# Performance work log

Measured on AMD Instinct MI355X. Metric: run time of the kernel, lower is better.

## Reference

```python
import jax, jax.numpy as jnp
import numpy as np

B, T, C = 2, 2048, 1024
NH = 16
HD = C // NH

def setup_inputs() -> dict:
    key = jax.random.key(0)
    k1, k2, k3 = jax.random.split(key, 3)
    x = jax.random.normal(k1, (B, T, C), dtype=jnp.float32)
    w_attn = jax.random.normal(k2, (C, 3 * C), dtype=jnp.float32) * 0.02
    w_proj = jax.random.normal(k3, (C, C), dtype=jnp.float32) * 0.02
    return {"x": x, "w_attn": w_attn, "w_proj": w_proj}

def reference(x, w_attn, w_proj):
    b, t, c = x.shape
    qkv = x @ w_attn                                  # [B,T,3C]
    q, k, v = jnp.split(qkv, 3, axis=-1)
    # [B,NH,T,HD]
    q = q.reshape(b, t, NH, HD).transpose(0, 2, 1, 3)
    k = k.reshape(b, t, NH, HD).transpose(0, 2, 1, 3)
    v = v.reshape(b, t, NH, HD).transpose(0, 2, 1, 3)
    scale = 1.0 / np.sqrt(HD).astype(np.float32)
    att = jnp.einsum('bhqd,bhkd->bhqk', q, k) * scale  # [B,NH,T,T]
    causal = jnp.tril(jnp.ones((t, t), dtype=bool))
    att = jnp.where(causal[None, None], att, jnp.float32(-jnp.inf))
    att = jax.nn.softmax(att, axis=-1)
    y = jnp.einsum('bhqk,bhkd->bhqd', att, v)          # [B,NH,T,HD]
    y = y.transpose(0, 2, 1, 3).reshape(b, t, c)
    return y @ w_proj
```

## Files before the change

kernel.cpp:

```cpp
#include <hip/hip_runtime.h>
#include <hip/hip_bf16.h>

#define BB 2
#define TT 2048
#define CCH 1024
#define NHH 16
#define HDD 64
#define M_TOK (BB*TT)
#define N_QKV (3*CCH)

typedef __attribute__((ext_vector_type(8))) short bf16x8;
typedef __attribute__((ext_vector_type(4))) float f32x4;
typedef unsigned short u16;
typedef unsigned int u32;

__device__ __forceinline__ u16 f2bf(float f) {
    union { float f; u32 u; } v; v.f = f;
    u32 u = v.u;
    u32 r = (u + 0x7FFFu + ((u >> 16) & 1u)) >> 16;
    return (u16)r;
}

__device__ __forceinline__ u32 pk_bf16(float a, float b) {
    u32 ua = __float_as_uint(a) + 0x8000u;
    u32 ub = __float_as_uint(b) + 0x8000u;
    return __builtin_amdgcn_perm(ub, ua, 0x07060302u);
}

__device__ __forceinline__ void async_copy16(const void* g, void* l) {
    __builtin_amdgcn_global_load_lds((__attribute__((address_space(1))) void*)g,
                                     (__attribute__((address_space(3))) void*)l,
                                     16, 0, 0);
}


__global__ __launch_bounds__(256) void cast_bf16_kernel(
    const float* __restrict__ src, u16* __restrict__ dst, int n4) {
    int i = blockIdx.x * 256 + threadIdx.x;
    if (i < n4) {
        float4 f = ((const float4*)src)[i];
        ushort4 o;
        o.x = f2bf(f.x); o.y = f2bf(f.y); o.z = f2bf(f.z); o.w = f2bf(f.w);
        ((ushort4*)dst)[i] = o;
    }
}

__global__ __launch_bounds__(256) void transpose_bf16_kernel(
    const float* __restrict__ src, u16* __restrict__ dst, int R, int Cn,
    int scale_rows, float sc) {
    __shared__ float tile[32][33];
    int c0 = blockIdx.x * 32, r0 = blockIdx.y * 32;
    int tx = threadIdx.x, ty = threadIdx.y;
#pragma unroll
    for (int i = ty; i < 32; i += 8)
        tile[i][tx] = src[(size_t)(r0 + i) * Cn + c0 + tx];
    __syncthreads();
#pragma unroll
    for (int i = ty; i < 32; i += 8) {
        float v = tile[tx][i];
        if (c0 + i < scale_rows) v *= sc;
        dst[(size_t)(c0 + i) * R + r0 + tx] = f2bf(v);
    }
}


#define QKV_NK 16
#define QKV_AS_HALF 16384
#define QKV_BS_HALF 12288
#define QKV_SMEM_BYTES ((2*QKV_AS_HALF + 2*QKV_BS_HALF) * 2)

__global__ __launch_bounds__(512, 1) void qkv_gemm_kernel(
    const u16* __restrict__ A, const u16* __restrict__ Bt,
    u16* __restrict__ Qo, u16* __restrict__ Ko, u16* __restrict__ Vto)
{
    extern __shared__ __align__(16) u16 smem[];
    u16* AsB = smem;
    u16* BsB = smem + 2 * QKV_AS_HALF;
    int t = threadIdx.x;
    int lane = t & 63, w = t >> 6;
    int m0 = blockIdx.y * 256, n0 = blockIdx.x * 192;
    int mw = (w >> 1) * 64, nw = (w & 1) * 96;
    int mr = lane & 15, quad = lane >> 4, swm = mr & 7;

    f32x4 zero = {0.f, 0.f, 0.f, 0.f};
    f32x4 acc[4][6];
#pragma unroll
    for (int i = 0; i < 4; ++i)
#pragma unroll
        for (int j = 0; j < 6; ++j) acc[i][j] = zero;

    int lr = lane >> 3;
    int cswz = (lane & 7) ^ lr;
    const u16* gA[4]; int lAo[4];
#pragma unroll
    for (int p = 0; p < 4; ++p) {
        int grp = w * 4 + p;
        gA[p] = A + (size_t)(m0 + grp * 8 + lr) * CCH + cswz * 8;
        lAo[p] = (grp * 64 + lane) * 8;
    }
    const u16* gB[3]; int lBo[3];
#pragma unroll
    for (int p = 0; p < 3; ++p) {
        int grp = w * 3 + p;
        gB[p] = Bt + (size_t)(n0 + grp * 8 + lr) * CCH + cswz * 8;
        lBo[p] = (grp * 64 + lane) * 8;
    }

#define QKV_STAGE(K0, BUF) do {                                               \
    u16* dA_ = AsB + (BUF) * QKV_AS_HALF;                                     \
    u16* dB_ = BsB + (BUF) * QKV_BS_HALF;                                     \
    _Pragma("unroll") for (int p_ = 0; p_ < 4; ++p_)                          \
        async_copy16(gA[p_] + (K0), dA_ + lAo[p_]);                           \
    _Pragma("unroll") for (int p_ = 0; p_ < 3; ++p_)                          \
        async_copy16(gB[p_] + (K0), dB_ + lBo[p_]);                           \
  } while (0)

    QKV_STAGE(0, 0);
    QKV_STAGE(64, 1);

    for (int k = 0; k < QKV_NK; ++k) {
        int cur = k & 1;
        if (k == QKV_NK - 1) asm volatile("s_waitcnt vmcnt(0)" ::: "memory");
        else                 asm volatile("s_waitcnt vmcnt(7)" ::: "memory");
        __builtin_amdgcn_s_barrier();
        asm volatile("" ::: "memory");
        const u16* Ac = AsB + cur * QKV_AS_HALF;
        const u16* Bc = BsB + cur * QKV_BS_HALF;
        bf16x8 a0[4], a1[4], b0[6], b1[6];
#pragma unroll
        for (int i = 0; i < 4; ++i) {
            int r = (mw + i * 16 + mr) * 64;
            a0[i] = *(const bf16x8*)&Ac[r + ((quad ^ swm) << 3)];
            a1[i] = *(const bf16x8*)&Ac[r + (((quad + 4) ^ swm) << 3)];
        }
#pragma unroll
        for (int j = 0; j < 6; ++j) {
            int r = (nw + j * 16 + mr) * 64;
            b0[j] = *(const bf16x8*)&Bc[r + ((quad ^ swm) << 3)];
            b1[j] = *(const bf16x8*)&Bc[r + (((quad + 4) ^ swm) << 3)];
        }
#pragma unroll
        for (int i = 0; i < 4; ++i)
#pragma unroll
            for (int j = 0; j < 6; ++j)
                acc[i][j] = __builtin_amdgcn_mfma_f32_16x16x32_bf16(b0[j], a0[i], acc[i][j], 0, 0, 0);
        asm volatile("s_waitcnt lgkmcnt(0)" ::: "memory");
        __builtin_amdgcn_sched_barrier(0);
        __builtin_amdgcn_s_barrier();
        asm volatile("" ::: "memory");
        if (k < QKV_NK - 2) QKV_STAGE((k + 2) * 64, cur);
#pragma unroll
        for (int i = 0; i < 4; ++i)
#pragma unroll
            for (int j = 0; j < 6; ++j)
                acc[i][j] = __builtin_amdgcn_mfma_f32_16x16x32_bf16(b1[j], a1[i], acc[i][j], 0, 0, 0);
    }
#undef QKV_STAGE

#pragma unroll
    for (int i = 0; i < 4; ++i)
#pragma unroll
        for (int j = 0; j < 6; ++j) {
            int tok = m0 + mw + i * 16 + mr;
            int cg0 = n0 + nw + j * 16 + quad * 4;
            int part = cg0 >> 10;
            int cc = cg0 & 1023;
            int h = cc >> 6, d0 = cc & 63;
            int b = tok >> 11, tt = tok & 2047;
            int bh = b * NHH + h;
            if (part < 2) {
                u16* dstp = part ? Ko : Qo;
                uint2 o;
                o.x = pk_bf16(acc[i][j][0], acc[i][j][1]);
                o.y = pk_bf16(acc[i][j][2], acc[i][j][3]);
                *(uint2*)&dstp[((size_t)bh * TT + tt) * HDD + d0] = o;
            } else {
#pragma unroll
                for (int r = 0; r < 4; ++r)
                    Vto[((size_t)bh * HDD + d0 + r) * TT + tt] = f2bf(acc[i][j][r]);
            }
        }
}


#define PRJ_NK 16
#define PRJ_AS_HALF 8192
#define PRJ_SMEM_BYTES (4 * PRJ_AS_HALF * 2)

__global__ __launch_bounds__(512, 1) void proj_gemm_kernel(
    const u16* __restrict__ A, const u16* __restrict__ Bt, float* __restrict__ Cout)
{
    extern __shared__ __align__(16) u16 psmem[];
    u16* AsB = psmem;
    u16* BsB = psmem + 2 * PRJ_AS_HALF;
    int t = threadIdx.x;
    int lane = t & 63, w = t >> 6;
    int m0 = blockIdx.y * 128, n0 = blockIdx.x * 128;
    int mw = (w >> 1) * 32, nw = (w & 1) * 64;
    int mr = lane & 15, quad = lane >> 4, swm = mr & 7;

    f32x4 zero = {0.f, 0.f, 0.f, 0.f};
    f32x4 acc[2][4];
#pragma unroll
    for (int i = 0; i < 2; ++i)
#pragma unroll
        for (int j = 0; j < 4; ++j) acc[i][j] = zero;

    int lr = lane >> 3;
    int cswz = (lane & 7) ^ lr;
    const u16* gA[2]; int lAo[2];
#pragma unroll
    for (int p = 0; p < 2; ++p) {
        int grp = w * 2 + p;
        gA[p] = A + (size_t)(m0 + grp * 8 + lr) * CCH + cswz * 8;
        lAo[p] = (grp * 64 + lane) * 8;
    }
    const u16* gB[2]; int lBo[2];
#pragma unroll
    for (int p = 0; p < 2; ++p) {
        int grp = w * 2 + p;
        gB[p] = Bt + (size_t)(n0 + grp * 8 + lr) * CCH + cswz * 8;
        lBo[p] = (grp * 64 + lane) * 8;
    }

#define PRJ_STAGE(K0, BUF) do {                                               \
    u16* dA_ = AsB + (BUF) * PRJ_AS_HALF;                                     \
    u16* dB_ = BsB + (BUF) * PRJ_AS_HALF;                                     \
    _Pragma("unroll") for (int p_ = 0; p_ < 2; ++p_)                          \
        async_copy16(gA[p_] + (K0), dA_ + lAo[p_]);                           \
    _Pragma("unroll") for (int p_ = 0; p_ < 2; ++p_)                          \
        async_copy16(gB[p_] + (K0), dB_ + lBo[p_]);                           \
  } while (0)

    PRJ_STAGE(0, 0);
    PRJ_STAGE(64, 1);

    for (int k = 0; k < PRJ_NK; ++k) {
        int cur = k & 1;
        if (k == PRJ_NK - 1) asm volatile("s_waitcnt vmcnt(0)" ::: "memory");
        else                 asm volatile("s_waitcnt vmcnt(4)" ::: "memory");
        __builtin_amdgcn_s_barrier();
        asm volatile("" ::: "memory");
        const u16* Ac = AsB + cur * PRJ_AS_HALF;
        const u16* Bc = BsB + cur * PRJ_AS_HALF;
        bf16x8 a0[2], a1[2], b0[4], b1[4];
#pragma unroll
        for (int i = 0; i < 2; ++i) {
            int r = (mw + i * 16 + mr) * 64;
            a0[i] = *(const bf16x8*)&Ac[r + ((quad ^ swm) << 3)];
            a1[i] = *(const bf16x8*)&Ac[r + (((quad + 4) ^ swm) << 3)];
        }
#pragma unroll
        for (int j = 0; j < 4; ++j) {
            int r = (nw + j * 16 + mr) * 64;
            b0[j] = *(const bf16x8*)&Bc[r + ((quad ^ swm) << 3)];
            b1[j] = *(const bf16x8*)&Bc[r + (((quad + 4) ^ swm) << 3)];
        }
#pragma unroll
        for (int i = 0; i < 2; ++i)
#pragma unroll
            for (int j = 0; j < 4; ++j)
                acc[i][j] = __builtin_amdgcn_mfma_f32_16x16x32_bf16(b0[j], a0[i], acc[i][j], 0, 0, 0);
        asm volatile("s_waitcnt lgkmcnt(0)" ::: "memory");
        __builtin_amdgcn_sched_barrier(0);
        __builtin_amdgcn_s_barrier();
        asm volatile("" ::: "memory");
        if (k < PRJ_NK - 2) PRJ_STAGE((k + 2) * 64, cur);
#pragma unroll
        for (int i = 0; i < 2; ++i)
#pragma unroll
            for (int j = 0; j < 4; ++j)
                acc[i][j] = __builtin_amdgcn_mfma_f32_16x16x32_bf16(b1[j], a1[i], acc[i][j], 0, 0, 0);
    }
#undef PRJ_STAGE

#pragma unroll
    for (int i = 0; i < 2; ++i)
#pragma unroll
        for (int j = 0; j < 4; ++j) {
            int tok = m0 + mw + i * 16 + mr;
            int cg0 = n0 + nw + j * 16 + quad * 4;
            float4 v;
            v.x = acc[i][j][0]; v.y = acc[i][j][1];
            v.z = acc[i][j][2]; v.w = acc[i][j][3];
            *(float4*)&Cout[(size_t)tok * CCH + cg0] = v;
        }
}


#define PST2 40

template<bool MASK>
__device__ __forceinline__ void tile3(
    const u16* __restrict__ Kb, const u16* __restrict__ Vb, u16* __restrict__ pb,
    bf16x8 qf0, bf16x8 qf1, bf16x8 ones, int m, int quad, int sw, int kh,
    int kvb, int qcol, f32x4 (&o)[4], f32x4& lacc)
{
    f32x4 zero = {0.f, 0.f, 0.f, 0.f};
#pragma unroll
    for (int kc = 0; kc < 2; ++kc) {
        int rr = kh * 32 + kc * 16 + m;
        bf16x8 kf0 = *(const bf16x8*)&Kb[rr * 64 + ((quad ^ sw) << 3)];
        bf16x8 kf1 = *(const bf16x8*)&Kb[rr * 64 + (((quad + 4) ^ sw) << 3)];
        f32x4 s  = __builtin_amdgcn_mfma_f32_16x16x32_bf16(kf0, qf0, zero, 0, 0, 0);
        f32x4 st = __builtin_amdgcn_mfma_f32_16x16x32_bf16(kf1, qf1, s, 0, 0, 0);
        float e0, e1, e2, e3;
#pragma unroll
        for (int r = 0; r < 4; ++r) {
            float v = st[r];
            if (MASK && (kvb + kc * 16 + quad * 4 + r > qcol)) v = -1e30f;
            float e = __builtin_amdgcn_exp2f(v);
            if (r == 0) e0 = e; else if (r == 1) e1 = e; else if (r == 2) e2 = e; else e3 = e;
        }
        uint2 pk; pk.x = pk_bf16(e0, e1); pk.y = pk_bf16(e2, e3);
        *(uint2*)&pb[m * PST2 + kc * 16 + quad * 4] = pk;
    }
    bf16x8 pf = *(const bf16x8*)&pb[m * PST2 + quad * 8];
    lacc = __builtin_amdgcn_mfma_f32_16x16x32_bf16(ones, pf, lacc, 0, 0, 0);
#pragma unroll
    for (int dg = 0; dg < 4; ++dg) {
        int rr = dg * 16 + m;
        bf16x8 vf = *(const bf16x8*)&Vb[rr * 64 + (((kh * 4 + quad) ^ sw) << 3)];
        o[dg] = __builtin_amdgcn_mfma_f32_16x16x32_bf16(vf, pf, o[dg], 0, 0, 0);
    }
}

#define SM_U16 26880

__global__ __launch_bounds__(512, 2) void attn_kernel(
    const u16* __restrict__ Q, const u16* __restrict__ K,
    const u16* __restrict__ Vt, u16* __restrict__ Y)
{
    __shared__ __align__(16) u16 smem[SM_U16];
    int t = threadIdx.x;
    int w = t >> 6, lane = t & 63;
    int m = lane & 15, quad = lane >> 4;
    int iq = w >> 1, kh = w & 1;

    int bid = blockIdx.x;
    int head = bid & 31;
    int g = bid >> 5;
    int pr = (g < 8) ? g : 23 - g;
    int qbA = pr;
    int qbB = 31 - pr;
    int rbA = qbA * 64 + iq * 16;
    int rbB = qbB * 64 + iq * 16;

    const u16* qpA = Q + ((size_t)head * TT + rbA + m) * HDD + quad * 8;
    const u16* qpB = Q + ((size_t)head * TT + rbB + m) * HDD + quad * 8;
    bf16x8 qA0 = *(const bf16x8*)qpA;
    bf16x8 qA1 = *(const bf16x8*)(qpA + 32);
    bf16x8 qB0 = *(const bf16x8*)qpB;
    bf16x8 qB1 = *(const bf16x8*)(qpB + 32);

    bf16x8 ones;
#pragma unroll
    for (int i = 0; i < 8; ++i) ones[i] = (short)0x3F80;

    const u16* kbase = K + (size_t)head * TT * HDD;
    const u16* vbase = Vt + (size_t)head * HDD * TT;
    u16* pbA = smem + 16384 + (w * 2 + 0) * (16 * PST2);
    u16* pbB = smem + 16384 + (w * 2 + 1) * (16 * PST2);

    int lr = lane >> 3;
    int cg = (lane & 7) ^ lr;
    int r0 = w * 8 + lr;
    int loff = (w * 64 + lane) * 8;

    f32x4 zero = {0.f, 0.f, 0.f, 0.f};
    f32x4 oA[4], oB[4], laA = zero, laB = zero;
#pragma unroll
    for (int dg = 0; dg < 4; ++dg) { oA[dg] = zero; oB[dg] = zero; }
    int qcA = rbA + m, qcB = rbB + m;
    int sw = m & 7;

    const u16* kst = kbase + (size_t)r0 * 64 + cg * 8;
    const u16* vst = vbase + (size_t)r0 * TT + cg * 8;

    async_copy16(kst, smem + loff);
    async_copy16(vst, smem + 8192 + loff);
    kst += 64 * HDD; vst += 64;

#define ATTN_CHUNK(KBUF, VBUF, IC) do {                                             \
    int kvb_ = ((IC) << 6) + kh * 32;                                               \
    if ((IC) < qbA)                                                                 \
        tile3<false>(KBUF, VBUF, pbA, qA0, qA1, ones, m, quad, sw, kh, kvb_, qcA, oA, laA); \
    else if ((IC) == qbA)                                                           \
        tile3<true >(KBUF, VBUF, pbA, qA0, qA1, ones, m, quad, sw, kh, kvb_, qcA, oA, laA); \
    if ((IC) < qbB)                                                                 \
        tile3<false>(KBUF, VBUF, pbB, qB0, qB1, ones, m, quad, sw, kh, kvb_, qcB, oB, laB); \
    else                                                                            \
        tile3<true >(KBUF, VBUF, pbB, qB0, qB1, ones, m, quad, sw, kh, kvb_, qcB, oB, laB); \
  } while (0)

    int ic = 0;
    while (ic + 1 <= qbB) {
        __syncthreads();
        async_copy16(kst, smem + 4096 + loff);
        async_copy16(vst, smem + 8192 + 4096 + loff);
        kst += 64 * HDD; vst += 64;
        ATTN_CHUNK(smem, smem + 8192, ic);
        __syncthreads();
        if (ic + 2 <= qbB) {
            async_copy16(kst, smem + loff);
            async_copy16(vst, smem + 8192 + loff);
            kst += 64 * HDD; vst += 64;
        }
        ATTN_CHUNK(smem + 4096, smem + 8192 + 4096, ic + 1);
        ic += 2;
    }
    if (ic <= qbB) {
        __syncthreads();
        ATTN_CHUNK(smem, smem + 8192, ic);
    }
#undef ATTN_CHUNK

    float lA = laA[0];
    float lB = laB[0];

    __syncthreads();
    f32x4* ob = (f32x4*)smem;
    float* lb = (float*)&smem[26624];
    if (kh) {
        f32x4* dst = ob + (size_t)iq * 512 + lane;
#pragma unroll
        for (int dg = 0; dg < 4; ++dg) {
            dst[dg * 64] = oA[dg];
            dst[(4 + dg) * 64] = oB[dg];
        }
        if (quad == 0) {
            lb[(iq * 2 + 0) * 16 + m] = lA;
            lb[(iq * 2 + 1) * 16 + m] = lB;
        }
    }
    __syncthreads();
    if (!kh) {
        f32x4* src = ob + (size_t)iq * 512 + lane;
#pragma unroll
        for (int dg = 0; dg < 4; ++dg) {
            oA[dg] += src[dg * 64];
            oB[dg] += src[(4 + dg) * 64];
        }
        lA += lb[(iq * 2 + 0) * 16 + m];
        lB += lb[(iq * 2 + 1) * 16 + m];
        float invA = 1.0f / lA, invB = 1.0f / lB;

        int b = head >> 4, h = head & 15;
        size_t roA = ((size_t)(b * TT + rbA + m)) * CCH + h * HDD;
        size_t roB = ((size_t)(b * TT + rbB + m)) * CCH + h * HDD;
#pragma unroll
        for (int dg = 0; dg < 4; ++dg) {
            uint2 ov;
            ov.x = pk_bf16(oA[dg][0] * invA, oA[dg][1] * invA);
            ov.y = pk_bf16(oA[dg][2] * invA, oA[dg][3] * invA);
            *(uint2*)&Y[roA + dg * 16 + quad * 4] = ov;
            ov.x = pk_bf16(oB[dg][0] * invB, oB[dg][1] * invB);
            ov.y = pk_bf16(oB[dg][2] * invB, oB[dg][3] * invB);
            *(uint2*)&Y[roB + dg * 16 + quad * 4] = ov;
        }
    }
}


extern "C" void kernel_launch(void* const* d_in, const int* in_sizes, int n_in,
                              void* d_out, int out_size, void* d_ws, size_t ws_size,
                              hipStream_t stream) {
    const float* x      = (const float*)d_in[0];
    const float* w_attn = (const float*)d_in[1];
    const float* w_proj = (const float*)d_in[2];
    float* out = (float*)d_out;

    char* ws = (char*)d_ws;
    u16* x_bf   = (u16*)ws; ws += (size_t)M_TOK * CCH * 2;
    u16* wqkvT  = (u16*)ws; ws += (size_t)N_QKV * CCH * 2;
    u16* wprojT = (u16*)ws; ws += (size_t)CCH * CCH * 2;
    u16* qbuf   = (u16*)ws; ws += (size_t)BB * NHH * TT * HDD * 2;
    u16* kbuf   = (u16*)ws; ws += (size_t)BB * NHH * TT * HDD * 2;
    u16* vtb    = (u16*)ws; ws += (size_t)BB * NHH * HDD * TT * 2;
    u16* yb     = (u16*)ws; ws += (size_t)M_TOK * CCH * 2;

    static bool attr_done = false;
    if (!attr_done) {
        (void)hipFuncSetAttribute(reinterpret_cast<const void*>(qkv_gemm_kernel),
                                  hipFuncAttributeMaxDynamicSharedMemorySize,
                                  QKV_SMEM_BYTES);
        (void)hipFuncSetAttribute(reinterpret_cast<const void*>(proj_gemm_kernel),
                                  hipFuncAttributeMaxDynamicSharedMemorySize,
                                  PRJ_SMEM_BYTES);
        attr_done = true;
    }

    const float QSC = 0.125f * 1.44269504088896f;

    cast_bf16_kernel<<<dim3(M_TOK * CCH / 4 / 256), dim3(256), 0, stream>>>(x, x_bf, M_TOK * CCH / 4);
    transpose_bf16_kernel<<<dim3(N_QKV / 32, CCH / 32), dim3(32, 8), 0, stream>>>(
        w_attn, wqkvT, CCH, N_QKV, CCH, QSC);
    transpose_bf16_kernel<<<dim3(CCH / 32, CCH / 32), dim3(32, 8), 0, stream>>>(
        w_proj, wprojT, CCH, CCH, 0, 1.0f);
    qkv_gemm_kernel<<<dim3(16, 16), dim3(512), QKV_SMEM_BYTES, stream>>>(
        x_bf, wqkvT, qbuf, kbuf, vtb);
    attn_kernel<<<dim3(512), dim3(512), 0, stream>>>(qbuf, kbuf, vtb, yb);
    proj_gemm_kernel<<<dim3(8, 32), dim3(512), PRJ_SMEM_BYTES, stream>>>(
        yb, wprojT, out);
}
```

Before: 170.9 us.

## Triple-buffer attention K/V tiles with explicit waitcnt and one barrier per chunk

The attention kernel's K/V staging moves from two shared-memory buffers to three, held in dynamic shared memory. Two tiles are prefetched before the loop. Each chunk does a partial vmcnt wait and a single raw s_barrier in place of two __syncthreads per pair of chunks. The intent is to keep two async loads in flight while computing, hiding global memory latency and cutting barrier stalls. Shared memory per block grows from about 53KB to about 70KB, which could limit the two-blocks-per-CU occupancy, and the hand-written waitcnt logic is fragile.

```diff
diff --git a/kernel.cpp b/kernel.cpp
--- a/kernel.cpp
+++ b/kernel.cpp
@@ -325,13 +325,14 @@
     }
 }
 
-#define SM_U16 26880
+#define ATTN_SM_U16 35072
+#define ATTN_SMEM_BYTES (ATTN_SM_U16 * 2)
 
 __global__ __launch_bounds__(512, 2) void attn_kernel(
     const u16* __restrict__ Q, const u16* __restrict__ K,
     const u16* __restrict__ Vt, u16* __restrict__ Y)
 {
-    __shared__ __align__(16) u16 smem[SM_U16];
+    extern __shared__ __align__(16) u16 asmem[];
     int t = threadIdx.x;
     int w = t >> 6, lane = t & 63;
     int m = lane & 15, quad = lane >> 4;
@@ -359,8 +360,8 @@
 
     const u16* kbase = K + (size_t)head * TT * HDD;
     const u16* vbase = Vt + (size_t)head * HDD * TT;
-    u16* pbA = smem + 16384 + (w * 2 + 0) * (16 * PST2);
-    u16* pbB = smem + 16384 + (w * 2 + 1) * (16 * PST2);
+    u16* pbA = asmem + 24576 + (w * 2 + 0) * (16 * PST2);
+    u16* pbB = asmem + 24576 + (w * 2 + 1) * (16 * PST2);
 
     int lr = lane >> 3;
     int cg = (lane & 7) ^ lr;
@@ -377,8 +378,11 @@
     const u16* kst = kbase + (size_t)r0 * 64 + cg * 8;
     const u16* vst = vbase + (size_t)r0 * TT + cg * 8;
 
-    async_copy16(kst, smem + loff);
-    async_copy16(vst, smem + 8192 + loff);
+    async_copy16(kst, asmem + loff);
+    async_copy16(vst, asmem + 12288 + loff);
+    kst += 64 * HDD; vst += 64;
+    async_copy16(kst, asmem + 4096 + loff);
+    async_copy16(vst, asmem + 16384 + loff);
     kst += 64 * HDD; vst += 64;
 
 #define ATTN_CHUNK(KBUF, VBUF, IC) do {                                             \
@@ -393,34 +397,43 @@
         tile3<true >(KBUF, VBUF, pbB, qB0, qB1, ones, m, quad, sw, kh, kvb_, qcB, oB, laB); \
   } while (0)
 
+#define ATTN_BODY(IC, KBUF, VBUF, PKBUF, PVBUF) do {                                \
+    if ((IC) < qbB) asm volatile("s_waitcnt vmcnt(2) lgkmcnt(0)" ::: "memory");     \
+    else            asm volatile("s_waitcnt vmcnt(0) lgkmcnt(0)" ::: "memory");     \
+    __builtin_amdgcn_s_barrier();                                                   \
+    asm volatile("" ::: "memory");                                                  \
+    if ((IC) + 2 <= qbB) {                                                          \
+        async_copy16(kst, (PKBUF) + loff);                                          \
+        async_copy16(vst, (PVBUF) + loff);                                          \
+        kst += 64 * HDD; vst += 64;                                                 \
+    }                                                                               \
+    ATTN_CHUNK(KBUF, VBUF, IC);                                                     \
+  } while (0)
+
     int ic = 0;
-    while (ic + 1 <= qbB) {
-        __syncthreads();
-        async_copy16(kst, smem + 4096 + loff);
-        async_copy16(vst, smem + 8192 + 4096 + loff);
-        kst += 64 * HDD; vst += 64;
-        ATTN_CHUNK(smem, smem + 8192, ic);
-        __syncthreads();
-        if (ic + 2 <= qbB) {
-            async_copy16(kst, smem + loff);
-            async_copy16(vst, smem + 8192 + loff);
-            kst += 64 * HDD; vst += 64;
-        }
-        ATTN_CHUNK(smem + 4096, smem + 8192 + 4096, ic + 1);
-        ic += 2;
+    while (ic + 2 <= qbB) {
+        ATTN_BODY(ic,     asmem,        asmem + 12288, asmem + 8192, asmem + 20480);
+        ATTN_BODY(ic + 1, asmem + 4096, asmem + 16384, asmem,        asmem + 12288);
+        ATTN_BODY(ic + 2, asmem + 8192, asmem + 20480, asmem + 4096, asmem + 16384);
+        ic += 3;
     }
     if (ic <= qbB) {
-        __syncthreads();
-        ATTN_CHUNK(smem, smem + 8192, ic);
-    }
+        ATTN_BODY(ic, asmem, asmem + 12288, asmem + 8192, asmem + 20480);
+        ++ic;
+    }
+    if (ic <= qbB) {
+        ATTN_BODY(ic, asmem + 4096, asmem + 16384, asmem, asmem + 12288);
+        ++ic;
+    }
+#undef ATTN_BODY
 #undef ATTN_CHUNK
 
     float lA = laA[0];
     float lB = laB[0];
 
     __syncthreads();
-    f32x4* ob = (f32x4*)smem;
-    float* lb = (float*)&smem[26624];
+    f32x4* ob = (f32x4*)asmem;
+    float* lb = (float*)&asmem[34816];
     if (kh) {
         f32x4* dst = ob + (size_t)iq * 512 + lane;
 #pragma unroll
@@ -487,6 +500,9 @@
         (void)hipFuncSetAttribute(reinterpret_cast<const void*>(proj_gemm_kernel),
                                   hipFuncAttributeMaxDynamicSharedMemorySize,
                                   PRJ_SMEM_BYTES);
+        (void)hipFuncSetAttribute(reinterpret_cast<const void*>(attn_kernel),
+                                  hipFuncAttributeMaxDynamicSharedMemorySize,
+                                  ATTN_SMEM_BYTES);
         attr_done = true;
     }
 
@@ -499,7 +515,7 @@
         w_proj, wprojT, CCH, CCH, 0, 1.0f);
     qkv_gemm_kernel<<<dim3(16, 16), dim3(512), QKV_SMEM_BYTES, stream>>>(
         x_bf, wqkvT, qbuf, kbuf, vtb);
-    attn_kernel<<<dim3(512), dim3(512), 0, stream>>>(qbuf, kbuf, vtb, yb);
+    attn_kernel<<<dim3(512), dim3(512), ATTN_SMEM_BYTES, stream>>>(qbuf, kbuf, vtb, yb);
     proj_gemm_kernel<<<dim3(8, 32), dim3(512), PRJ_SMEM_BYTES, stream>>>(
         yb, wprojT, out);
 }
```

Result: faster. 166.7 us (-2.5%).
